# Optimization experiments

Hardware: AMD Instinct MI355X
Metric: run time of the kernel (lower is better)

Reference implementation:

```python
import jax, jax.numpy as jnp
import numpy as np

# Architecture constants (match init_kwargs)
STEPS, BATCH = 256, 128
IN_SIZE, H1, H2, OUT = 512, 1536, 1536, 512
DELAY = 1


def setup_inputs() -> dict:
    key = jax.random.key(0)
    ks = jax.random.split(key, 5)
    def init_w(k, shape):
        fan_in = shape[0]
        return (jax.random.normal(k, shape, jnp.float32) / np.sqrt(fan_in).astype(np.float32))
    return {
        "inputs": jax.random.normal(ks[0], (STEPS, BATCH, IN_SIZE), jnp.float32),
        # hidden1 RNNC: in = sizes['#input'] + sizes['hidden1'] (self-recurrent conn)
        "W1": init_w(ks[1], (IN_SIZE + H1, H1)),
        "b1": jnp.zeros((H1,), jnp.float32),
        # hidden2 RNNC: in = sizes['hidden1'] + sizes['hidden2']
        "W2": init_w(ks[2], (H1 + H2, H2)),
        "b2": jnp.zeros((H2,), jnp.float32),
        # '##output' PlaceholderWt: linear readout from hidden2
        "Wo": init_w(ks[3], (H2, OUT)),
        "bo": jnp.zeros((OUT,), jnp.float32),
    }


def reference(inputs, W1, b1, W2, b2, Wo, bo):
    # Stepped multi-layer RNN with delay=1 spike buffers.
    # Within a step, layers update in order, so a layer reading spikes_all[-1]
    # of an EARLIER layer sees the current step's spike, while self/backward
    # connections see the previous step's spike (carried through the scan).
    B = inputs.shape[1]

    def step(carry, x_t):
        s_h1_prev, s_h2_prev = carry
        s_in = x_t                                               # Placeholder '#input'
        # hidden1: prevs = ['#input' (current), 'hidden1' (prev step)]
        s_h1 = jnp.tanh(jnp.concatenate([s_in, s_h1_prev], -1) @ W1 + b1)
        # hidden2: prevs = ['hidden1' (current), 'hidden2' (prev step)]
        s_h2 = jnp.tanh(jnp.concatenate([s_h1, s_h2_prev], -1) @ W2 + b2)
        # '##output' PlaceholderWt: linear readout of current hidden2 spike
        out = s_h2 @ Wo + bo
        return (s_h1, s_h2), out

    init = (jnp.zeros((B, H1), inputs.dtype), jnp.zeros((B, H2), inputs.dtype))
    _, outs = jax.lax.scan(step, init, inputs)                   # [steps, B, OUT]
    # spikes_all includes `delay` initial zero spikes from reset_state
    zeros = jnp.zeros((DELAY, B, OUT), inputs.dtype)
    return jnp.concatenate([zeros, outs], axis=0)                # [delay+steps, B, OUT]
```

## Files before the change

### kernel.cpp

```cpp
#include <hip/hip_runtime.h>
#include <math.h>

#define STEPS 256
#define BATCH 128
#define HALF_M 64
#define INSZ  512
#define H1SZ  1536
#define H2SZ  1536
#define NOUT  512
#define K1    2048
#define K2    3072
#define NC1   48
#define NC2   48
#define NC3   16
#define NBLK  224

typedef short bf16x8 __attribute__((ext_vector_type(8)));
typedef float f32x4  __attribute__((ext_vector_type(4)));
typedef unsigned short u16;

__device__ __forceinline__ f32x4 mfma16(bf16x8 a, bf16x8 b, f32x4 c) {
  return __builtin_amdgcn_mfma_f32_16x16x32_bf16(a, b, c, 0, 0, 0);
}

__device__ __forceinline__ u16 f2bf(float f) {
  unsigned u = __builtin_bit_cast(unsigned, f);
  u += 0x7fffu + ((u >> 16) & 1u);
  return (u16)(u >> 16);
}

__device__ __forceinline__ bf16x8 cvt8(const float* p) {
  f32x4 lo = *(const f32x4*)p;
  f32x4 hi = *(const f32x4*)(p + 4);
  union { unsigned u[4]; bf16x8 v; } r;
  asm("v_cvt_pk_bf16_f32 %0, %1, %2" : "=v"(r.u[0]) : "v"(lo[0]), "v"(lo[1]));
  asm("v_cvt_pk_bf16_f32 %0, %1, %2" : "=v"(r.u[1]) : "v"(lo[2]), "v"(lo[3]));
  asm("v_cvt_pk_bf16_f32 %0, %1, %2" : "=v"(r.u[2]) : "v"(hi[0]), "v"(hi[1]));
  asm("v_cvt_pk_bf16_f32 %0, %1, %2" : "=v"(r.u[3]) : "v"(hi[2]), "v"(hi[3]));
  return r.v;
}

#define LOAD_SC_OFS(dst, ptr, ofs) \
  asm volatile("global_load_dwordx4 %0, %1, off offset:%2 sc0 sc1" \
               : "=v"(dst) : "v"(ptr), "i"(ofs) : "memory")
#define STORE_SC(ptr, val) \
  asm volatile("global_store_dwordx4 %0, %1, off sc0 sc1" :: "v"(ptr), "v"(val) : "memory")
#define WAITV(n) asm volatile("s_waitcnt vmcnt(" #n ")" ::: "memory")
#define PIN4(v) asm volatile("" : "+v"(v))

__device__ __forceinline__ void wait_flag(const int* p, int v) {
  while (__hip_atomic_load(p, __ATOMIC_RELAXED, __HIP_MEMORY_SCOPE_SYSTEM) < v)
    __builtin_amdgcn_s_sleep(1);
}
__device__ __forceinline__ void set_flag(int* p, int v) {
  __hip_atomic_store(p, v, __ATOMIC_RELAXED, __HIP_MEMORY_SCOPE_SYSTEM);
}

template<int NKS>
__device__ __forceinline__ void kloop_sc(const u16* base, const bf16x8 (*Br)[2],
                                         f32x4 (*acc)[2], int r16) {
  const u16* rp[4];
#pragma unroll
  for (int mf = 0; mf < 4; ++mf) rp[mf] = base + (size_t)(mf * 16 + r16) * 1536;
  bf16x8 A[8][4];
  WAITV(0);
  constexpr int D = (NKS < 8) ? NKS : 8;
#pragma unroll
  for (int d = 0; d < D; ++d)
#pragma unroll
    for (int mf = 0; mf < 4; ++mf)
      LOAD_SC_OFS(A[d][mf], rp[mf], d * 64);
#pragma unroll
  for (int ks = 0; ks < NKS; ++ks) {
    const int rem = (NKS - 1 - ks) < 7 ? (NKS - 1 - ks) : 7;
    if (rem == 7)      WAITV(28);
    else if (rem == 6) WAITV(24);
    else if (rem == 5) WAITV(20);
    else if (rem == 4) WAITV(16);
    else if (rem == 3) WAITV(12);
    else if (rem == 2) WAITV(8);
    else if (rem == 1) WAITV(4);
    else               WAITV(0);
    __builtin_amdgcn_sched_barrier(0);
#pragma unroll
    for (int mf = 0; mf < 4; ++mf) {
      acc[mf][0] = mfma16(A[ks & 7][mf], Br[ks][0], acc[mf][0]);
      acc[mf][1] = mfma16(A[ks & 7][mf], Br[ks][1], acc[mf][1]);
    }
    if (ks + 8 < NKS) {
#pragma unroll
      for (int mf = 0; mf < 4; ++mf)
        LOAD_SC_OFS(A[ks & 7][mf], rp[mf], (ks + 8) * 64);
    }
  }
}

__device__ __forceinline__ void kloop_x4(const float* xb, const bf16x8 (*Br)[2],
                                         f32x4 (*acc)[2], int r16) {
#pragma unroll
  for (int ks = 0; ks < 4; ++ks)
#pragma unroll
    for (int mf = 0; mf < 4; ++mf) {
      bf16x8 a = cvt8(xb + (size_t)(mf * 16 + r16) * INSZ + ks * 32);
      acc[mf][0] = mfma16(a, Br[ks][0], acc[mf][0]);
      acc[mf][1] = mfma16(a, Br[ks][1], acc[mf][1]);
    }
}

__device__ __forceinline__ void store_red(float (*red)[64][36], int kw, int kg, int r16,
                                          const f32x4 (*acc)[2]) {
#pragma unroll
  for (int mf = 0; mf < 4; ++mf)
#pragma unroll
    for (int nf = 0; nf < 2; ++nf)
#pragma unroll
      for (int r = 0; r < 4; ++r)
        red[kw][mf * 16 + kg * 4 + r][nf * 16 + r16] = acc[mf][nf][r];
}

__device__ __forceinline__ void reduce_tanh_sc(const float (*red)[64][36], const float* bias,
                                               u16* dstbase, int n0, int tid) {
  const int row = tid >> 2, c0 = (tid & 3) * 8;
  f32x4 s0 = *(const f32x4*)(bias + n0 + c0);
  f32x4 s1 = *(const f32x4*)(bias + n0 + c0 + 4);
#pragma unroll
  for (int w = 0; w < 4; ++w) {
    s0 += *(const f32x4*)&red[w][row][c0];
    s1 += *(const f32x4*)&red[w][row][c0 + 4];
  }
  float t[8];
#pragma unroll
  for (int j = 0; j < 4; ++j) t[j] = tanhf(s0[j]);
#pragma unroll
  for (int j = 0; j < 4; ++j) t[4 + j] = tanhf(s1[j]);
  union { unsigned u[4]; bf16x8 v; } pk;
  asm("v_cvt_pk_bf16_f32 %0, %1, %2" : "=v"(pk.u[0]) : "v"(t[0]), "v"(t[1]));
  asm("v_cvt_pk_bf16_f32 %0, %1, %2" : "=v"(pk.u[1]) : "v"(t[2]), "v"(t[3]));
  asm("v_cvt_pk_bf16_f32 %0, %1, %2" : "=v"(pk.u[2]) : "v"(t[4]), "v"(t[5]));
  asm("v_cvt_pk_bf16_f32 %0, %1, %2" : "=v"(pk.u[3]) : "v"(t[6]), "v"(t[7]));
  u16* dst = dstbase + (size_t)row * 1536 + n0 + c0;
  STORE_SC(dst, pk.v);
}

__global__ __launch_bounds__(256, 1) void rnn_main(
    const float* __restrict__ x,
    const u16* __restrict__ W1T, const u16* __restrict__ W2T, const u16* __restrict__ WoT,
    const float* __restrict__ b1, const float* __restrict__ b2, const float* __restrict__ bo,
    u16* __restrict__ h1ring, u16* __restrict__ h2ring,
    float* __restrict__ out, int* __restrict__ bar)
{
  __shared__ float red[4][64][36];
  const int tid = threadIdx.x;
  const int kw = tid >> 6, lane = tid & 63;
  const int r16 = lane & 15, kg = lane >> 4;
  const int bid = blockIdx.x;

  int grp, half, col;
  if (bid < 2 * NC1)              { grp = 0; half = bid / NC1;         col = bid % NC1; }
  else if (bid < 2 * (NC1 + NC2)) { grp = 1; half = (bid - 96) / NC2;  col = (bid - 96) % NC2; }
  else                            { grp = 2; half = (bid - 192) / NC3; col = (bid - 192) % NC3; }
  const int n0 = col * 32;
  int* f1 = bar + (half * NC1) * 16;
  int* f2 = bar + (96 + half * NC2) * 16;
  int* f3 = bar + (192 + half * NC3) * 16;

  u16* h1base = h1ring + (size_t)half * 4 * HALF_M * H1SZ;
  u16* h2base = h2ring + (size_t)half * 4 * HALF_M * H2SZ;

  if (grp == 0) {
    bf16x8 BrX[4][2], Brh[12][2];
#pragma unroll
    for (int ks = 0; ks < 4; ++ks)
#pragma unroll
      for (int nf = 0; nf < 2; ++nf)
        BrX[ks][nf] = *(const bf16x8*)(W1T + (size_t)(n0 + nf * 16 + r16) * K1
                                       + kw * 128 + ks * 32 + kg * 8);
#pragma unroll
    for (int ks = 0; ks < 12; ++ks)
#pragma unroll
      for (int nf = 0; nf < 2; ++nf)
        Brh[ks][nf] = *(const bf16x8*)(W1T + (size_t)(n0 + nf * 16 + r16) * K1
                                       + 512 + kw * 384 + ks * 32 + kg * 8);
#pragma unroll
    for (int ks = 0; ks < 4; ++ks) { PIN4(BrX[ks][0]); PIN4(BrX[ks][1]); }
#pragma unroll
    for (int ks = 0; ks < 12; ++ks) { PIN4(Brh[ks][0]); PIN4(Brh[ks][1]); }

    for (int k = 0; k < STEPS; ++k) {
      if (tid < NC1) wait_flag(&f1[tid * 16], k);
      else if (tid >= 64 && tid < 64 + NC2) wait_flag(&f2[(tid - 64) * 16], k - 3);
      __syncthreads();
      f32x4 acc[4][2] = {};
      const float* xb = x + ((size_t)k * BATCH + half * HALF_M) * INSZ + kw * 128 + kg * 8;
      kloop_x4(xb, BrX, acc, r16);
      const u16* hb = h1base + (size_t)((k + 3) & 3) * HALF_M * H1SZ + kw * 384 + kg * 8;
      kloop_sc<12>(hb, Brh, acc, r16);
      store_red(red, kw, kg, r16, acc);
      __syncthreads();
      reduce_tanh_sc(red, b1, h1base + (size_t)(k & 3) * HALF_M * H1SZ, n0, tid);
      WAITV(0);
      __syncthreads();
      if (tid == 0) set_flag(&f1[col * 16], k + 1);
    }
  } else if (grp == 1) {
    bf16x8 Br[24][2];
#pragma unroll
    for (int ks = 0; ks < 24; ++ks)
#pragma unroll
      for (int nf = 0; nf < 2; ++nf)
        Br[ks][nf] = *(const bf16x8*)(W2T + (size_t)(n0 + nf * 16 + r16) * K2
                                      + kw * 768 + ks * 32 + kg * 8);
#pragma unroll
    for (int ks = 0; ks < 24; ++ks) { PIN4(Br[ks][0]); PIN4(Br[ks][1]); }

    for (int j = 0; j < STEPS; ++j) {
      if (tid < NC1) wait_flag(&f1[tid * 16], j + 1);
      else if (tid >= 64 && tid < 64 + NC2) wait_flag(&f2[(tid - 64) * 16], j);
      else if (tid >= 128 && tid < 128 + NC3) wait_flag(&f3[(tid - 128) * 16], j - 3);
      __syncthreads();
      const u16* hb = (kw < 2)
        ? h1base + (size_t)(j & 3) * HALF_M * H1SZ + kw * 768 + kg * 8
        : h2base + (size_t)((j + 3) & 3) * HALF_M * H2SZ + (kw - 2) * 768 + kg * 8;
      f32x4 acc[4][2] = {};
      kloop_sc<24>(hb, Br, acc, r16);
      store_red(red, kw, kg, r16, acc);
      __syncthreads();
      reduce_tanh_sc(red, b2, h2base + (size_t)(j & 3) * HALF_M * H2SZ, n0, tid);
      WAITV(0);
      __syncthreads();
      if (tid == 0) set_flag(&f2[col * 16], j + 1);
    }
  } else {
    bf16x8 Br[12][2];
#pragma unroll
    for (int ks = 0; ks < 12; ++ks)
#pragma unroll
      for (int nf = 0; nf < 2; ++nf)
        Br[ks][nf] = *(const bf16x8*)(WoT + (size_t)(n0 + nf * 16 + r16) * H2SZ
                                      + kw * 384 + ks * 32 + kg * 8);
#pragma unroll
    for (int ks = 0; ks < 12; ++ks) { PIN4(Br[ks][0]); PIN4(Br[ks][1]); }

    for (int j = 0; j < STEPS; ++j) {
      if (tid < NC2) wait_flag(&f2[tid * 16], j + 1);
      __syncthreads();
      const u16* hb = h2base + (size_t)(j & 3) * HALF_M * H2SZ + kw * 384 + kg * 8;
      f32x4 acc[4][2] = {};
      kloop_sc<12>(hb, Br, acc, r16);
      store_red(red, kw, kg, r16, acc);
      __syncthreads();
      {
        const int row = tid >> 2, c0 = (tid & 3) * 8;
        f32x4 s0 = *(const f32x4*)(bo + n0 + c0);
        f32x4 s1 = *(const f32x4*)(bo + n0 + c0 + 4);
#pragma unroll
        for (int w = 0; w < 4; ++w) {
          s0 += *(const f32x4*)&red[w][row][c0];
          s1 += *(const f32x4*)&red[w][row][c0 + 4];
        }
        float* dst = out + ((size_t)(j + 1) * BATCH + half * HALF_M + row) * NOUT + n0 + c0;
        *(f32x4*)dst = s0;
        *(f32x4*)(dst + 4) = s1;
      }
      __syncthreads();
      if (tid == 0) set_flag(&f3[col * 16], j + 1);
    }
  }
}

__global__ void transpose_cvt(const float* __restrict__ src, u16* __restrict__ dst, int K, int N) {
  __shared__ u16 tile[32][33];
  int kb = blockIdx.x * 32, nb = blockIdx.y * 32;
  int tx = threadIdx.x & 31, ty = threadIdx.x >> 5;
  for (int i = ty; i < 32; i += 8)
    tile[i][tx] = f2bf(src[(size_t)(kb + i) * N + nb + tx]);
  __syncthreads();
  for (int i = ty; i < 32; i += 8)
    dst[(size_t)(nb + i) * K + kb + tx] = tile[tx][i];
}

extern "C" void kernel_launch(void* const* d_in, const int* in_sizes, int n_in,
                              void* d_out, int out_size, void* d_ws, size_t ws_size,
                              hipStream_t stream) {
  const float* x  = (const float*)d_in[0];
  const float* W1 = (const float*)d_in[1];
  const float* b1 = (const float*)d_in[2];
  const float* W2 = (const float*)d_in[3];
  const float* b2 = (const float*)d_in[4];
  const float* Wo = (const float*)d_in[5];
  const float* bo = (const float*)d_in[6];
  float* out = (float*)d_out;
  char*  ws  = (char*)d_ws;

  u16* W1T    = (u16*)(ws);
  u16* W2T    = (u16*)(ws + 6291456);
  u16* WoT    = (u16*)(ws + 15728640);
  u16* h1ring = (u16*)(ws + 17301504);
  u16* h2ring = (u16*)(ws + 18874368);
  int* bar    = (int*)(ws + 20447232);

  hipMemsetAsync(ws + 17301504, 0, 1572864 * 2 + 14336, stream);
  hipMemsetAsync(d_out, 0, (size_t)BATCH * NOUT * sizeof(float), stream);

  transpose_cvt<<<dim3(K1 / 32, H1SZ / 32), 256, 0, stream>>>(W1, W1T, K1, H1SZ);
  transpose_cvt<<<dim3(K2 / 32, H1SZ / 32), 256, 0, stream>>>(W2, W2T, K2, H1SZ);
  transpose_cvt<<<dim3(H2SZ / 32, NOUT / 32), 256, 0, stream>>>(Wo, WoT, H2SZ, NOUT);

  rnn_main<<<NBLK, 256, 0, stream>>>(x, W1T, W2T, WoT, b1, b2, bo, h1ring, h2ring, out, bar);
}
```

Measured before the change: 3.489 ms.

## Split K across eight waves per block to halve per-wave serial GEMM work

Doubles the block to 512 threads (8 waves) and splits each layer's K dimension across eight waves instead of four, so each wave holds half as many weight fragments and runs half as many MFMA k-steps per timestep. For layer 1, two waves now handle the fp32 input part and six the recurrent h1 part. The LDS reduction buffer grows to 8 partial sums, the epilogue is reshaped to 4 columns per thread, and bias loads are hoisted out of the step loop. The prefetch depth drops from 8 to 6 to ease register pressure. The aim is to shorten the latency-bound critical path of each recurrent step, at the cost of a larger reduction and more waves per CU.

```diff
diff --git a/kernel.cpp b/kernel.cpp
--- a/kernel.cpp
+++ b/kernel.cpp
@@ -17,6 +17,7 @@
 
 typedef short bf16x8 __attribute__((ext_vector_type(8)));
 typedef float f32x4  __attribute__((ext_vector_type(4)));
+typedef unsigned u32x2 __attribute__((ext_vector_type(2)));
 typedef unsigned short u16;
 
 __device__ __forceinline__ f32x4 mfma16(bf16x8 a, bf16x8 b, f32x4 c) {
@@ -43,8 +44,8 @@
 #define LOAD_SC_OFS(dst, ptr, ofs) \
   asm volatile("global_load_dwordx4 %0, %1, off offset:%2 sc0 sc1" \
                : "=v"(dst) : "v"(ptr), "i"(ofs) : "memory")
-#define STORE_SC(ptr, val) \
-  asm volatile("global_store_dwordx4 %0, %1, off sc0 sc1" :: "v"(ptr), "v"(val) : "memory")
+#define STORE_SC2(ptr, val) \
+  asm volatile("global_store_dwordx2 %0, %1, off sc0 sc1" :: "v"(ptr), "v"(val) : "memory")
 #define WAITV(n) asm volatile("s_waitcnt vmcnt(" #n ")" ::: "memory")
 #define PIN4(v) asm volatile("" : "+v"(v))
 
@@ -57,14 +58,14 @@
 }
 
 template<int NKS>
-__device__ __forceinline__ void kloop_sc(const u16* base, const bf16x8 (*Br)[2],
-                                         f32x4 (*acc)[2], int r16) {
+__device__ __forceinline__ void kloop8(const u16* base, int rstride,
+                                       const bf16x8 (*Br)[2], f32x4 (*acc)[2], int r16) {
   const u16* rp[4];
 #pragma unroll
-  for (int mf = 0; mf < 4; ++mf) rp[mf] = base + (size_t)(mf * 16 + r16) * 1536;
-  bf16x8 A[8][4];
+  for (int mf = 0; mf < 4; ++mf) rp[mf] = base + (size_t)(mf * 16 + r16) * rstride;
+  bf16x8 A[6][4];
   WAITV(0);
-  constexpr int D = (NKS < 8) ? NKS : 8;
+  constexpr int D = (NKS < 6) ? NKS : 6;
 #pragma unroll
   for (int d = 0; d < D; ++d)
 #pragma unroll
@@ -72,10 +73,8 @@
       LOAD_SC_OFS(A[d][mf], rp[mf], d * 64);
 #pragma unroll
   for (int ks = 0; ks < NKS; ++ks) {
-    const int rem = (NKS - 1 - ks) < 7 ? (NKS - 1 - ks) : 7;
-    if (rem == 7)      WAITV(28);
-    else if (rem == 6) WAITV(24);
-    else if (rem == 5) WAITV(20);
+    const int rem = (NKS - 1 - ks) < (D - 1) ? (NKS - 1 - ks) : (D - 1);
+    if (rem == 5)      WAITV(20);
     else if (rem == 4) WAITV(16);
     else if (rem == 3) WAITV(12);
     else if (rem == 2) WAITV(8);
@@ -84,21 +83,21 @@
     __builtin_amdgcn_sched_barrier(0);
 #pragma unroll
     for (int mf = 0; mf < 4; ++mf) {
-      acc[mf][0] = mfma16(A[ks & 7][mf], Br[ks][0], acc[mf][0]);
-      acc[mf][1] = mfma16(A[ks & 7][mf], Br[ks][1], acc[mf][1]);
-    }
-    if (ks + 8 < NKS) {
+      acc[mf][0] = mfma16(A[ks % 6][mf], Br[ks][0], acc[mf][0]);
+      acc[mf][1] = mfma16(A[ks % 6][mf], Br[ks][1], acc[mf][1]);
+    }
+    if (ks + 6 < NKS) {
 #pragma unroll
       for (int mf = 0; mf < 4; ++mf)
-        LOAD_SC_OFS(A[ks & 7][mf], rp[mf], (ks + 8) * 64);
+        LOAD_SC_OFS(A[ks % 6][mf], rp[mf], (ks + 6) * 64);
     }
   }
 }
 
-__device__ __forceinline__ void kloop_x4(const float* xb, const bf16x8 (*Br)[2],
+__device__ __forceinline__ void kloop_x8(const float* xb, const bf16x8 (*Br)[2],
                                          f32x4 (*acc)[2], int r16) {
 #pragma unroll
-  for (int ks = 0; ks < 4; ++ks)
+  for (int ks = 0; ks < 8; ++ks)
 #pragma unroll
     for (int mf = 0; mf < 4; ++mf) {
       bf16x8 a = cvt8(xb + (size_t)(mf * 16 + r16) * INSZ + ks * 32);
@@ -118,38 +117,28 @@
         red[kw][mf * 16 + kg * 4 + r][nf * 16 + r16] = acc[mf][nf][r];
 }
 
-__device__ __forceinline__ void reduce_tanh_sc(const float (*red)[64][36], const float* bias,
-                                               u16* dstbase, int n0, int tid) {
-  const int row = tid >> 2, c0 = (tid & 3) * 8;
-  f32x4 s0 = *(const f32x4*)(bias + n0 + c0);
-  f32x4 s1 = *(const f32x4*)(bias + n0 + c0 + 4);
-#pragma unroll
-  for (int w = 0; w < 4; ++w) {
-    s0 += *(const f32x4*)&red[w][row][c0];
-    s1 += *(const f32x4*)&red[w][row][c0 + 4];
-  }
-  float t[8];
-#pragma unroll
-  for (int j = 0; j < 4; ++j) t[j] = tanhf(s0[j]);
-#pragma unroll
-  for (int j = 0; j < 4; ++j) t[4 + j] = tanhf(s1[j]);
-  union { unsigned u[4]; bf16x8 v; } pk;
-  asm("v_cvt_pk_bf16_f32 %0, %1, %2" : "=v"(pk.u[0]) : "v"(t[0]), "v"(t[1]));
-  asm("v_cvt_pk_bf16_f32 %0, %1, %2" : "=v"(pk.u[1]) : "v"(t[2]), "v"(t[3]));
-  asm("v_cvt_pk_bf16_f32 %0, %1, %2" : "=v"(pk.u[2]) : "v"(t[4]), "v"(t[5]));
-  asm("v_cvt_pk_bf16_f32 %0, %1, %2" : "=v"(pk.u[3]) : "v"(t[6]), "v"(t[7]));
+__device__ __forceinline__ void epi_tanh(const float (*red)[64][36], f32x4 biasv,
+                                         u16* dstbase, int n0, int tid) {
+  const int row = tid >> 3, c0 = (tid & 7) * 4;
+  f32x4 s = biasv;
+#pragma unroll
+  for (int w = 0; w < 8; ++w) s += *(const f32x4*)&red[w][row][c0];
+  float t0 = tanhf(s[0]), t1 = tanhf(s[1]), t2 = tanhf(s[2]), t3 = tanhf(s[3]);
+  u32x2 pk;
+  asm("v_cvt_pk_bf16_f32 %0, %1, %2" : "=v"(pk[0]) : "v"(t0), "v"(t1));
+  asm("v_cvt_pk_bf16_f32 %0, %1, %2" : "=v"(pk[1]) : "v"(t2), "v"(t3));
   u16* dst = dstbase + (size_t)row * 1536 + n0 + c0;
-  STORE_SC(dst, pk.v);
-}
-
-__global__ __launch_bounds__(256, 1) void rnn_main(
+  STORE_SC2(dst, pk);
+}
+
+__global__ __launch_bounds__(512, 1) void rnn_main(
     const float* __restrict__ x,
     const u16* __restrict__ W1T, const u16* __restrict__ W2T, const u16* __restrict__ WoT,
     const float* __restrict__ b1, const float* __restrict__ b2, const float* __restrict__ bo,
     u16* __restrict__ h1ring, u16* __restrict__ h2ring,
     float* __restrict__ out, int* __restrict__ bar)
 {
-  __shared__ float red[4][64][36];
+  __shared__ float red[8][64][36];
   const int tid = threadIdx.x;
   const int kw = tid >> 6, lane = tid & 63;
   const int r16 = lane & 15, kg = lane >> 4;
@@ -168,99 +157,93 @@
   u16* h2base = h2ring + (size_t)half * 4 * HALF_M * H2SZ;
 
   if (grp == 0) {
-    bf16x8 BrX[4][2], Brh[12][2];
-#pragma unroll
-    for (int ks = 0; ks < 4; ++ks)
+    bf16x8 Br[8][2];
+#pragma unroll
+    for (int ks = 0; ks < 8; ++ks)
 #pragma unroll
       for (int nf = 0; nf < 2; ++nf)
-        BrX[ks][nf] = *(const bf16x8*)(W1T + (size_t)(n0 + nf * 16 + r16) * K1
-                                       + kw * 128 + ks * 32 + kg * 8);
-#pragma unroll
-    for (int ks = 0; ks < 12; ++ks)
-#pragma unroll
-      for (int nf = 0; nf < 2; ++nf)
-        Brh[ks][nf] = *(const bf16x8*)(W1T + (size_t)(n0 + nf * 16 + r16) * K1
-                                       + 512 + kw * 384 + ks * 32 + kg * 8);
-#pragma unroll
-    for (int ks = 0; ks < 4; ++ks) { PIN4(BrX[ks][0]); PIN4(BrX[ks][1]); }
-#pragma unroll
-    for (int ks = 0; ks < 12; ++ks) { PIN4(Brh[ks][0]); PIN4(Brh[ks][1]); }
+        Br[ks][nf] = *(const bf16x8*)(W1T + (size_t)(n0 + nf * 16 + r16) * K1
+                                      + kw * 256 + ks * 32 + kg * 8);
+#pragma unroll
+    for (int ks = 0; ks < 8; ++ks) { PIN4(Br[ks][0]); PIN4(Br[ks][1]); }
+    const f32x4 biasv = *(const f32x4*)(b1 + n0 + (tid & 7) * 4);
 
     for (int k = 0; k < STEPS; ++k) {
       if (tid < NC1) wait_flag(&f1[tid * 16], k);
       else if (tid >= 64 && tid < 64 + NC2) wait_flag(&f2[(tid - 64) * 16], k - 3);
       __syncthreads();
       f32x4 acc[4][2] = {};
-      const float* xb = x + ((size_t)k * BATCH + half * HALF_M) * INSZ + kw * 128 + kg * 8;
-      kloop_x4(xb, BrX, acc, r16);
-      const u16* hb = h1base + (size_t)((k + 3) & 3) * HALF_M * H1SZ + kw * 384 + kg * 8;
-      kloop_sc<12>(hb, Brh, acc, r16);
+      if (kw < 2) {
+        const float* xb = x + ((size_t)k * BATCH + half * HALF_M) * INSZ + kw * 256 + kg * 8;
+        kloop_x8(xb, Br, acc, r16);
+      } else {
+        const u16* hb = h1base + (size_t)((k + 3) & 3) * HALF_M * H1SZ
+                        + (kw - 2) * 256 + kg * 8;
+        kloop8<8>(hb, H1SZ, Br, acc, r16);
+      }
       store_red(red, kw, kg, r16, acc);
       __syncthreads();
-      reduce_tanh_sc(red, b1, h1base + (size_t)(k & 3) * HALF_M * H1SZ, n0, tid);
+      epi_tanh(red, biasv, h1base + (size_t)(k & 3) * HALF_M * H1SZ, n0, tid);
       WAITV(0);
       __syncthreads();
       if (tid == 0) set_flag(&f1[col * 16], k + 1);
     }
   } else if (grp == 1) {
-    bf16x8 Br[24][2];
-#pragma unroll
-    for (int ks = 0; ks < 24; ++ks)
+    bf16x8 Br[12][2];
+#pragma unroll
+    for (int ks = 0; ks < 12; ++ks)
 #pragma unroll
       for (int nf = 0; nf < 2; ++nf)
         Br[ks][nf] = *(const bf16x8*)(W2T + (size_t)(n0 + nf * 16 + r16) * K2
-                                      + kw * 768 + ks * 32 + kg * 8);
-#pragma unroll
-    for (int ks = 0; ks < 24; ++ks) { PIN4(Br[ks][0]); PIN4(Br[ks][1]); }
+                                      + kw * 384 + ks * 32 + kg * 8);
+#pragma unroll
+    for (int ks = 0; ks < 12; ++ks) { PIN4(Br[ks][0]); PIN4(Br[ks][1]); }
+    const f32x4 biasv = *(const f32x4*)(b2 + n0 + (tid & 7) * 4);
 
     for (int j = 0; j < STEPS; ++j) {
       if (tid < NC1) wait_flag(&f1[tid * 16], j + 1);
       else if (tid >= 64 && tid < 64 + NC2) wait_flag(&f2[(tid - 64) * 16], j);
       else if (tid >= 128 && tid < 128 + NC3) wait_flag(&f3[(tid - 128) * 16], j - 3);
       __syncthreads();
-      const u16* hb = (kw < 2)
-        ? h1base + (size_t)(j & 3) * HALF_M * H1SZ + kw * 768 + kg * 8
-        : h2base + (size_t)((j + 3) & 3) * HALF_M * H2SZ + (kw - 2) * 768 + kg * 8;
+      const u16* hb = (kw < 4)
+        ? h1base + (size_t)(j & 3) * HALF_M * H1SZ + kw * 384 + kg * 8
+        : h2base + (size_t)((j + 3) & 3) * HALF_M * H2SZ + (kw - 4) * 384 + kg * 8;
       f32x4 acc[4][2] = {};
-      kloop_sc<24>(hb, Br, acc, r16);
+      kloop8<12>(hb, 1536, Br, acc, r16);
       store_red(red, kw, kg, r16, acc);
       __syncthreads();
-      reduce_tanh_sc(red, b2, h2base + (size_t)(j & 3) * HALF_M * H2SZ, n0, tid);
+      epi_tanh(red, biasv, h2base + (size_t)(j & 3) * HALF_M * H2SZ, n0, tid);
       WAITV(0);
       __syncthreads();
       if (tid == 0) set_flag(&f2[col * 16], j + 1);
     }
   } else {
-    bf16x8 Br[12][2];
-#pragma unroll
-    for (int ks = 0; ks < 12; ++ks)
+    bf16x8 Br[6][2];
+#pragma unroll
+    for (int ks = 0; ks < 6; ++ks)
 #pragma unroll
       for (int nf = 0; nf < 2; ++nf)
         Br[ks][nf] = *(const bf16x8*)(WoT + (size_t)(n0 + nf * 16 + r16) * H2SZ
-                                      + kw * 384 + ks * 32 + kg * 8);
-#pragma unroll
-    for (int ks = 0; ks < 12; ++ks) { PIN4(Br[ks][0]); PIN4(Br[ks][1]); }
+                                      + kw * 192 + ks * 32 + kg * 8);
+#pragma unroll
+    for (int ks = 0; ks < 6; ++ks) { PIN4(Br[ks][0]); PIN4(Br[ks][1]); }
+    const f32x4 biasv = *(const f32x4*)(bo + n0 + (tid & 7) * 4);
 
     for (int j = 0; j < STEPS; ++j) {
       if (tid < NC2) wait_flag(&f2[tid * 16], j + 1);
       __syncthreads();
-      const u16* hb = h2base + (size_t)(j & 3) * HALF_M * H2SZ + kw * 384 + kg * 8;
+      const u16* hb = h2base + (size_t)(j & 3) * HALF_M * H2SZ + kw * 192 + kg * 8;
       f32x4 acc[4][2] = {};
-      kloop_sc<12>(hb, Br, acc, r16);
+      kloop8<6>(hb, 1536, Br, acc, r16);
       store_red(red, kw, kg, r16, acc);
       __syncthreads();
       {
-        const int row = tid >> 2, c0 = (tid & 3) * 8;
-        f32x4 s0 = *(const f32x4*)(bo + n0 + c0);
-        f32x4 s1 = *(const f32x4*)(bo + n0 + c0 + 4);
-#pragma unroll
-        for (int w = 0; w < 4; ++w) {
-          s0 += *(const f32x4*)&red[w][row][c0];
-          s1 += *(const f32x4*)&red[w][row][c0 + 4];
-        }
+        const int row = tid >> 3, c0 = (tid & 7) * 4;
+        f32x4 s = biasv;
+#pragma unroll
+        for (int w = 0; w < 8; ++w) s += *(const f32x4*)&red[w][row][c0];
         float* dst = out + ((size_t)(j + 1) * BATCH + half * HALF_M + row) * NOUT + n0 + c0;
-        *(f32x4*)dst = s0;
-        *(f32x4*)(dst + 4) = s1;
+        *(f32x4*)dst = s;
       }
       __syncthreads();
       if (tid == 0) set_flag(&f3[col * 16], j + 1);
@@ -306,5 +289,5 @@
   transpose_cvt<<<dim3(K2 / 32, H1SZ / 32), 256, 0, stream>>>(W2, W2T, K2, H1SZ);
   transpose_cvt<<<dim3(H2SZ / 32, NOUT / 32), 256, 0, stream>>>(Wo, WoT, H2SZ, NOUT);
 
-  rnn_main<<<NBLK, 256, 0, stream>>>(x, W1T, W2T, WoT, b1, b2, bo, h1ring, h2ring, out, bar);
-}
+  rnn_main<<<NBLK, 512, 0, stream>>>(x, W1T, W2T, WoT, b1, b2, bo, h1ring, h2ring, out, bar);
+}
```

Result: slower. 4.243 ms (+21.6%).

## Replace block-wide flag waits with per-wave waits on only needed producer columns

Applied to the files above, without the earlier changes.

Each wave now polls only the flags of the producer blocks whose output columns it actually reads, using a wave-wide any-vote, instead of a few threads polling every flag followed by a block barrier. Layer 2 splits its K loop so the recurrent h2 half runs before waiting for the current h1 step, which overlaps that work with layer-1 latency. Bias values are hoisted out of the step loop. The finer-grained dependency tracking must exactly match the K-slice each wave reads, which is a correctness risk, and skipping the block barrier lets waves drift apart within a step.

```diff
diff --git a/kernel.cpp b/kernel.cpp
--- a/kernel.cpp
+++ b/kernel.cpp
@@ -48,31 +48,33 @@
 #define WAITV(n) asm volatile("s_waitcnt vmcnt(" #n ")" ::: "memory")
 #define PIN4(v) asm volatile("" : "+v"(v))
 
-__device__ __forceinline__ void wait_flag(const int* p, int v) {
-  while (__hip_atomic_load(p, __ATOMIC_RELAXED, __HIP_MEMORY_SCOPE_SYSTEM) < v)
-    __builtin_amdgcn_s_sleep(1);
-}
 __device__ __forceinline__ void set_flag(int* p, int v) {
   __hip_atomic_store(p, v, __ATOMIC_RELAXED, __HIP_MEMORY_SCOPE_SYSTEM);
 }
 
-template<int NKS>
-__device__ __forceinline__ void kloop_sc(const u16* base, const bf16x8 (*Br)[2],
-                                         f32x4 (*acc)[2], int r16) {
+__device__ __forceinline__ void wave_wait(const int* p, int tgt, bool active) {
+  while (true) {
+    int v = __hip_atomic_load(p, __ATOMIC_RELAXED, __HIP_MEMORY_SCOPE_SYSTEM);
+    if (!__any(active && (v < tgt))) break;
+    __builtin_amdgcn_s_sleep(1);
+  }
+}
+
+__device__ __forceinline__ void kloop12(const u16* base, const bf16x8 (*Br)[2],
+                                        f32x4 (*acc)[2], int r16) {
   const u16* rp[4];
 #pragma unroll
   for (int mf = 0; mf < 4; ++mf) rp[mf] = base + (size_t)(mf * 16 + r16) * 1536;
   bf16x8 A[8][4];
   WAITV(0);
-  constexpr int D = (NKS < 8) ? NKS : 8;
-#pragma unroll
-  for (int d = 0; d < D; ++d)
+#pragma unroll
+  for (int d = 0; d < 8; ++d)
 #pragma unroll
     for (int mf = 0; mf < 4; ++mf)
       LOAD_SC_OFS(A[d][mf], rp[mf], d * 64);
 #pragma unroll
-  for (int ks = 0; ks < NKS; ++ks) {
-    const int rem = (NKS - 1 - ks) < 7 ? (NKS - 1 - ks) : 7;
+  for (int ks = 0; ks < 12; ++ks) {
+    const int rem = (11 - ks) < 7 ? (11 - ks) : 7;
     if (rem == 7)      WAITV(28);
     else if (rem == 6) WAITV(24);
     else if (rem == 5) WAITV(20);
@@ -87,7 +89,7 @@
       acc[mf][0] = mfma16(A[ks & 7][mf], Br[ks][0], acc[mf][0]);
       acc[mf][1] = mfma16(A[ks & 7][mf], Br[ks][1], acc[mf][1]);
     }
-    if (ks + 8 < NKS) {
+    if (ks < 4) {
 #pragma unroll
       for (int mf = 0; mf < 4; ++mf)
         LOAD_SC_OFS(A[ks & 7][mf], rp[mf], (ks + 8) * 64);
@@ -118,11 +120,10 @@
         red[kw][mf * 16 + kg * 4 + r][nf * 16 + r16] = acc[mf][nf][r];
 }
 
-__device__ __forceinline__ void reduce_tanh_sc(const float (*red)[64][36], const float* bias,
-                                               u16* dstbase, int n0, int tid) {
+__device__ __forceinline__ void epi_tanh(const float (*red)[64][36], f32x4 bv0, f32x4 bv1,
+                                         u16* dstbase, int n0, int tid) {
   const int row = tid >> 2, c0 = (tid & 3) * 8;
-  f32x4 s0 = *(const f32x4*)(bias + n0 + c0);
-  f32x4 s1 = *(const f32x4*)(bias + n0 + c0 + 4);
+  f32x4 s0 = bv0, s1 = bv1;
 #pragma unroll
   for (int w = 0; w < 4; ++w) {
     s0 += *(const f32x4*)&red[w][row][c0];
@@ -142,7 +143,9 @@
   STORE_SC(dst, pk.v);
 }
 
-__global__ __launch_bounds__(256, 1) void rnn_main(
+__global__ __launch_bounds__(256)
+__attribute__((amdgpu_waves_per_eu(1, 1)))
+void rnn_main(
     const float* __restrict__ x,
     const u16* __restrict__ W1T, const u16* __restrict__ W2T, const u16* __restrict__ WoT,
     const float* __restrict__ b1, const float* __restrict__ b2, const float* __restrict__ bo,
@@ -167,6 +170,22 @@
   u16* h1base = h1ring + (size_t)half * 4 * HALF_M * H1SZ;
   u16* h2base = h2ring + (size_t)half * 4 * HALF_M * H2SZ;
 
+  const int* wpA = f1; int dA = 0; bool aA = false;
+  const int* wpB = f1; int dB = 0; bool aB = false;
+  if (grp == 0) {
+    if (lane < 12)                      { wpA = f1 + (kw * 12 + lane) * 16; dA = 0;  aA = true; }
+    else if (kw == 0 && lane >= 16)     { wpA = f2 + (lane - 16) * 16;      dA = -3; aA = true; }
+  } else if (grp == 1) {
+    if (lane < 12) {
+      wpA = f2 + (kw * 12 + lane) * 16; dA = 0; aA = true;
+      wpB = f1 + (kw * 12 + lane) * 16; dB = 1; aB = true;
+    } else if (kw == 0 && lane >= 32 && lane < 48) {
+      wpA = f3 + (lane - 32) * 16; dA = -3; aA = true;
+    }
+  } else {
+    if (lane < 12)                      { wpA = f2 + (kw * 12 + lane) * 16; dA = 1;  aA = true; }
+  }
+
   if (grp == 0) {
     bf16x8 BrX[4][2], Brh[12][2];
 #pragma unroll
@@ -185,47 +204,51 @@
     for (int ks = 0; ks < 4; ++ks) { PIN4(BrX[ks][0]); PIN4(BrX[ks][1]); }
 #pragma unroll
     for (int ks = 0; ks < 12; ++ks) { PIN4(Brh[ks][0]); PIN4(Brh[ks][1]); }
+    const f32x4 bv0 = *(const f32x4*)(b1 + n0 + (tid & 3) * 8);
+    const f32x4 bv1 = *(const f32x4*)(b1 + n0 + (tid & 3) * 8 + 4);
 
     for (int k = 0; k < STEPS; ++k) {
-      if (tid < NC1) wait_flag(&f1[tid * 16], k);
-      else if (tid >= 64 && tid < 64 + NC2) wait_flag(&f2[(tid - 64) * 16], k - 3);
-      __syncthreads();
       f32x4 acc[4][2] = {};
       const float* xb = x + ((size_t)k * BATCH + half * HALF_M) * INSZ + kw * 128 + kg * 8;
       kloop_x4(xb, BrX, acc, r16);
-      const u16* hb = h1base + (size_t)((k + 3) & 3) * HALF_M * H1SZ + kw * 384 + kg * 8;
-      kloop_sc<12>(hb, Brh, acc, r16);
+      wave_wait(wpA, k + dA, aA);
+      kloop12(h1base + (size_t)((k + 3) & 3) * HALF_M * H1SZ + kw * 384 + kg * 8,
+              Brh, acc, r16);
       store_red(red, kw, kg, r16, acc);
       __syncthreads();
-      reduce_tanh_sc(red, b1, h1base + (size_t)(k & 3) * HALF_M * H1SZ, n0, tid);
+      epi_tanh(red, bv0, bv1, h1base + (size_t)(k & 3) * HALF_M * H1SZ, n0, tid);
       WAITV(0);
       __syncthreads();
       if (tid == 0) set_flag(&f1[col * 16], k + 1);
     }
   } else if (grp == 1) {
-    bf16x8 Br[24][2];
-#pragma unroll
-    for (int ks = 0; ks < 24; ++ks)
-#pragma unroll
-      for (int nf = 0; nf < 2; ++nf)
-        Br[ks][nf] = *(const bf16x8*)(W2T + (size_t)(n0 + nf * 16 + r16) * K2
-                                      + kw * 768 + ks * 32 + kg * 8);
-#pragma unroll
-    for (int ks = 0; ks < 24; ++ks) { PIN4(Br[ks][0]); PIN4(Br[ks][1]); }
+    bf16x8 Bh2[12][2], Bh1[12][2];
+#pragma unroll
+    for (int ks = 0; ks < 12; ++ks)
+#pragma unroll
+      for (int nf = 0; nf < 2; ++nf) {
+        Bh2[ks][nf] = *(const bf16x8*)(W2T + (size_t)(n0 + nf * 16 + r16) * K2
+                                       + 1536 + kw * 384 + ks * 32 + kg * 8);
+        Bh1[ks][nf] = *(const bf16x8*)(W2T + (size_t)(n0 + nf * 16 + r16) * K2
+                                       + kw * 384 + ks * 32 + kg * 8);
+      }
+#pragma unroll
+    for (int ks = 0; ks < 12; ++ks) { PIN4(Bh2[ks][0]); PIN4(Bh2[ks][1]);
+                                      PIN4(Bh1[ks][0]); PIN4(Bh1[ks][1]); }
+    const f32x4 bv0 = *(const f32x4*)(b2 + n0 + (tid & 3) * 8);
+    const f32x4 bv1 = *(const f32x4*)(b2 + n0 + (tid & 3) * 8 + 4);
 
     for (int j = 0; j < STEPS; ++j) {
-      if (tid < NC1) wait_flag(&f1[tid * 16], j + 1);
-      else if (tid >= 64 && tid < 64 + NC2) wait_flag(&f2[(tid - 64) * 16], j);
-      else if (tid >= 128 && tid < 128 + NC3) wait_flag(&f3[(tid - 128) * 16], j - 3);
-      __syncthreads();
-      const u16* hb = (kw < 2)
-        ? h1base + (size_t)(j & 3) * HALF_M * H1SZ + kw * 768 + kg * 8
-        : h2base + (size_t)((j + 3) & 3) * HALF_M * H2SZ + (kw - 2) * 768 + kg * 8;
       f32x4 acc[4][2] = {};
-      kloop_sc<24>(hb, Br, acc, r16);
+      wave_wait(wpA, j + dA, aA);
+      kloop12(h2base + (size_t)((j + 3) & 3) * HALF_M * H2SZ + kw * 384 + kg * 8,
+              Bh2, acc, r16);
+      wave_wait(wpB, j + dB, aB);
+      kloop12(h1base + (size_t)(j & 3) * HALF_M * H1SZ + kw * 384 + kg * 8,
+              Bh1, acc, r16);
       store_red(red, kw, kg, r16, acc);
       __syncthreads();
-      reduce_tanh_sc(red, b2, h2base + (size_t)(j & 3) * HALF_M * H2SZ, n0, tid);
+      epi_tanh(red, bv0, bv1, h2base + (size_t)(j & 3) * HALF_M * H2SZ, n0, tid);
       WAITV(0);
       __syncthreads();
       if (tid == 0) set_flag(&f2[col * 16], j + 1);
@@ -240,19 +263,19 @@
                                       + kw * 384 + ks * 32 + kg * 8);
 #pragma unroll
     for (int ks = 0; ks < 12; ++ks) { PIN4(Br[ks][0]); PIN4(Br[ks][1]); }
+    const f32x4 bv0 = *(const f32x4*)(bo + n0 + (tid & 3) * 8);
+    const f32x4 bv1 = *(const f32x4*)(bo + n0 + (tid & 3) * 8 + 4);
 
     for (int j = 0; j < STEPS; ++j) {
-      if (tid < NC2) wait_flag(&f2[tid * 16], j + 1);
-      __syncthreads();
-      const u16* hb = h2base + (size_t)(j & 3) * HALF_M * H2SZ + kw * 384 + kg * 8;
       f32x4 acc[4][2] = {};
-      kloop_sc<12>(hb, Br, acc, r16);
+      wave_wait(wpA, j + dA, aA);
+      kloop12(h2base + (size_t)(j & 3) * HALF_M * H2SZ + kw * 384 + kg * 8,
+              Br, acc, r16);
       store_red(red, kw, kg, r16, acc);
       __syncthreads();
       {
         const int row = tid >> 2, c0 = (tid & 3) * 8;
-        f32x4 s0 = *(const f32x4*)(bo + n0 + c0);
-        f32x4 s1 = *(const f32x4*)(bo + n0 + c0 + 4);
+        f32x4 s0 = bv0, s1 = bv1;
 #pragma unroll
         for (int w = 0; w < 4; ++w) {
           s0 += *(const f32x4*)&red[w][row][c0];
```

Result: no change. 3.544 ms (+1.6%).
